# Optimization experiments

Hardware: AMD Instinct MI355X
Metric: run time of the kernel (lower is better)

## Reference

```python
import jax, jax.numpy as jnp
import numpy as np

DT = 0.05        # Euler step size
S_EULER = 2      # Euler steps between consecutive events, and after the last one (prop_to_end)


def setup_inputs() -> dict:
    key = jax.random.key(0)
    B, H, D, K, E = 512, 512, 128, 64, 256
    ks = jax.random.split(key, 16)

    def w(k, fan_in, fan_out):
        return jax.random.normal(k, (fan_in, fan_out), jnp.float32) / np.float32(np.sqrt(fan_in))

    X = jax.random.normal(ks[0], (K, E, D), jnp.float32)
    M = jax.random.bernoulli(ks[1], 0.5, (K, E, D)).astype(jnp.float32)
    # unique sample indices per event (irregular observation pattern, no scatter collisions)
    batch_idx = jax.vmap(lambda k: jax.random.permutation(k, B)[:E])(jax.random.split(ks[2], K))
    sample_idx = jnp.arange(B)
    b = lambda n: jnp.full((n,), 0.01, jnp.float32)  # torch init: bias filled with 0.01
    return {
        'X': X, 'M': M, 'batch_idx': batch_idx, 'sample_idx': sample_idx,
        'Wi': w(ks[3], D + H, H), 'bi': b(H),
        'Wf': w(ks[4], D + H, H), 'bf': b(H),
        'Wo': w(ks[5], D + H, H), 'bo': b(H),
        'Wc': w(ks[6], D + H, H), 'bc': b(H),
        'W1': w(ks[7], H, H), 'b1': b(H),
        'W2': w(ks[8], H, H), 'b2': b(H),
        'Wp1': w(ks[9], H, H), 'bp1': b(H),
        'Wp2': w(ks[10], H, D), 'bp2': b(D),
    }


def reference(X, M, batch_idx, sample_idx,
              Wi, bi, Wf, bf, Wo, bo, Wc, bc,
              W1, b1, W2, b2, Wp1, bp1, Wp2, bp2):
    B = sample_idx.shape[0]
    H = W1.shape[0]
    h0 = jnp.zeros((B, H), X.dtype)
    c0 = jnp.zeros((B, H), X.dtype)

    def euler(h):  # h <- h + dt * ODEFunc(h)
        return h + DT * (jnp.tanh(h @ W1 + b1) @ W2 + b2)

    def p_model(h):  # Linear -> ReLU -> (Dropout p=0, eval) -> Linear
        return jax.nn.relu(h @ Wp1 + bp1) @ Wp2 + bp2

    def step(carry, xs):
        h, c, loss, tot_m = carry
        Xo, Mo, idx = xs  # [E,D], [E,D], [E]
        for _ in range(S_EULER):
            h = euler(h)
        p = p_model(h)
        loss = loss + jnp.sum(jnp.abs(Xo - p[idx]) * Mo)
        tot_m = tot_m + jnp.sum(Mo)
        inp = jnp.concatenate([Xo, h[idx]], axis=-1)  # [E, D+H]
        ig = jax.nn.sigmoid(inp @ Wi + bi)
        fg = jax.nn.sigmoid(inp @ Wf + bf)
        og = jax.nn.sigmoid(inp @ Wo + bo)
        ct = jnp.tanh(inp @ Wc + bc)
        c_new = fg * c[idx] + ig * ct
        h_new = og * jnp.tanh(c_new)
        return (h.at[idx].set(h_new), c.at[idx].set(c_new), loss, tot_m), None

    init = (h0, c0, jnp.float32(0.0), jnp.float32(0.0))
    (h, c, loss, tot_m), _ = jax.lax.scan(step, init, (X, M, batch_idx))
    for _ in range(S_EULER):  # prop_to_end up to T
        h = euler(h)
    return jnp.stack([loss, loss / tot_m])
```

## Files before the change

kernel.cpp:

```cpp
#include <hip/hip_runtime.h>
#include <hip/hip_fp16.h>
#include <stdint.h>

#define Kn 64
#define En 256
#define Bn 512
#define Hn 512
#define Dn 128
#define NBLK 256
#define NTH  256
#define DT_C 0.05f


typedef _Float16 f16x8 __attribute__((ext_vector_type(8)));
typedef float    f32x4 __attribute__((ext_vector_type(4)));
typedef unsigned long long u64;

__device__ __forceinline__ float sigm(float x){ return 1.0f/(1.0f + __expf(-x)); }

__device__ __forceinline__ u64 ald(const u64* p){
  return __hip_atomic_load(p, __ATOMIC_RELAXED, __HIP_MEMORY_SCOPE_AGENT);
}
__device__ __forceinline__ void ast(u64* p, u64 v){
  __hip_atomic_store(p, v, __ATOMIC_RELAXED, __HIP_MEMORY_SCOPE_AGENT);
}

union HU { __half h[8]; u64 q[2]; uint32_t w[4]; };

__global__ void k_init(int* __restrict__ pos, float* __restrict__ acc,
                       int* __restrict__ ctr, uint32_t* __restrict__ hf){
  int i = blockIdx.x*blockDim.x + threadIdx.x;
  if (i < Kn*Bn) pos[i] = -1;
  if (i < 2) acc[i] = 0.0f;
  if (i < 1024) ctr[i] = 0;
  if (i < Hn*Hn/2) hf[i] = 0;
}

__global__ void k_scatter(const int* __restrict__ bidx, int* __restrict__ pos){
  int i = blockIdx.x*blockDim.x + threadIdx.x;
  if (i < Kn*En){
    int k = i >> 8;
    int e = i & (En-1);
    pos[(k << 9) | bidx[i]] = e;
  }
}

__global__ void k_cvt_frag(const float* __restrict__ src, __half* __restrict__ dst,
                           int KT, int N, int n){
  int i = blockIdx.x*blockDim.x + threadIdx.x;
  if (i >= n) return;
  int C = i / (KT*512);
  int r = i % (KT*512);
  int T = r >> 9;
  int q = r & 511;
  int l = q >> 3, e = q & 7;
  int srow = T*32 + ((l>>4)<<3) + e;
  int scol = C*16 + (l&15);
  dst[i] = __float2half(src[(size_t)srow*N + scol]);
}

__device__ __forceinline__ void gsync(int* c, int tgt){
  asm volatile("s_waitcnt vmcnt(0)" ::: "memory");
  __syncthreads();
  if (threadIdx.x == 0){
    __hip_atomic_fetch_add(c, 1, __ATOMIC_RELAXED, __HIP_MEMORY_SCOPE_AGENT);
    while (__hip_atomic_load(c, __ATOMIC_RELAXED, __HIP_MEMORY_SCOPE_AGENT) < tgt)
      __builtin_amdgcn_s_sleep(1);
  }
  __syncthreads();
}

__global__ __launch_bounds__(NTH, 1) void k_main(
  const float* __restrict__ X, const float* __restrict__ Mm,
  const int* __restrict__ pos, const __half* __restrict__ WF,
  __half* __restrict__ Hf, __half* __restrict__ Tf,
  const float* __restrict__ bi_, const float* __restrict__ bf_,
  const float* __restrict__ bo_, const float* __restrict__ bc_,
  const float* __restrict__ b1_, const float* __restrict__ b2_,
  const float* __restrict__ bp1_, const float* __restrict__ bp2_,
  float* __restrict__ acc, int* __restrict__ ctrbase)
{
  const __half* W1F  = WF;
  const __half* W2F  = WF + 262144;
  const __half* Wp1F = WF + 524288;
  const __half* Wp2F = WF + 786432;
  const __half* WgF  = WF + 851968;

  const int t    = threadIdx.x;
  const int bid  = blockIdx.x;
  const int s    = bid & 7;
  const int g    = bid >> 3;
  const int w    = t >> 6;
  const int lane = t & 63;

  int* ctr = ctrbase + g*32;

  __shared__ __align__(16) __half Afrag[16*512];
  __shared__ __align__(16) __half Xfrag[4*512];
  __shared__ __align__(16) float  outb[20*256];
  __shared__ float redbuf[8];

  const int row = t >> 4;
  const int q4  = t & 15;
  const int sc  = s*64 + q4*4;
  float Hreg[4] = {0,0,0,0};
  float Creg[4] = {0,0,0,0};
  float vb1[4], vb2[4], vbp1[4], vbi[4], vbf[4], vbo[4], vbc[4];
  #pragma unroll
  for (int i=0;i<4;i++){
    vb1[i]=b1_[sc+i]; vb2[i]=b2_[sc+i]; vbp1[i]=bp1_[sc+i];
    vbi[i]=bi_[sc+i]; vbf[i]=bf_[sc+i]; vbo[i]=bo_[sc+i]; vbc[i]=bc_[sc+i];
  }
  const float vbp2 = bp2_[s*16 + q4];

  f16x8 W1r[16], W2r[16], Wp1r[16];
  {
    const size_t cb = (size_t)(s*4 + w)*16*512 + lane*8;
    #pragma unroll
    for (int kt=0; kt<16; kt++){
      W1r[kt]  = *(const f16x8*)(W1F  + cb + kt*512);
      W2r[kt]  = *(const f16x8*)(W2F  + cb + kt*512);
      Wp1r[kt] = *(const f16x8*)(Wp1F + cb + kt*512);
    }
  }

  float loss_loc = 0.f, m_loc = 0.f;
  int round = 0;
  const int grow = g*16 + row;

  for (int k=0; k<Kn; k++){
    const int epos = pos[(k<<9) + grow];

    #pragma unroll 1
    for (int ph=0; ph<4; ph++){
      const __half* src = (ph & 1) ? Tf : Hf;
      {
        const int ar = t & 15, ch = t >> 4;
        const u64* sp = (const u64*)(src + ((size_t)(g*16+ar))*512 + ch*32);
        u64 v[8];
        #pragma unroll
        for (int i=0;i<8;i++) v[i] = ald(sp+i);
        #pragma unroll
        for (int kg=0;kg<4;kg++){
          u64* d = (u64*)(Afrag + ch*512 + (ar + 16*kg)*8);
          d[0] = v[2*kg]; d[1] = v[2*kg+1];
        }
      }
      __syncthreads();
      {
        f32x4 a4 = {0,0,0,0};
        if (!(ph & 1)){
          #pragma unroll
          for (int kt=0; kt<16; kt++){
            f16x8 a = *(const f16x8*)(Afrag + kt*512 + lane*8);
            a4 = __builtin_amdgcn_mfma_f32_16x16x32_f16(a, W1r[kt], a4, 0,0,0);
          }
        } else {
          #pragma unroll
          for (int kt=0; kt<16; kt++){
            f16x8 a = *(const f16x8*)(Afrag + kt*512 + lane*8);
            a4 = __builtin_amdgcn_mfma_f32_16x16x32_f16(a, W2r[kt], a4, 0,0,0);
          }
        }
        float* o = outb + w*256 + ((lane>>4)*4)*16 + (lane&15);
        o[0]=a4[0]; o[16]=a4[1]; o[32]=a4[2]; o[48]=a4[3];
      }
      __syncthreads();
      {
        const float* o = outb + (q4>>2)*256 + row*16 + (q4&3)*4;
        float v0=o[0], v1=o[1], v2=o[2], v3=o[3];
        HU u;
        if (!(ph & 1)){
          u.h[0]=__float2half(tanhf(v0+vb1[0])); u.h[1]=__float2half(tanhf(v1+vb1[1]));
          u.h[2]=__float2half(tanhf(v2+vb1[2])); u.h[3]=__float2half(tanhf(v3+vb1[3]));
          ast((u64*)(Tf + (size_t)grow*512 + sc), u.q[0]);
        } else {
          Hreg[0] += DT_C*(v0+vb2[0]); Hreg[1] += DT_C*(v1+vb2[1]);
          Hreg[2] += DT_C*(v2+vb2[2]); Hreg[3] += DT_C*(v3+vb2[3]);
          u.h[0]=__float2half(Hreg[0]); u.h[1]=__float2half(Hreg[1]);
          u.h[2]=__float2half(Hreg[2]); u.h[3]=__float2half(Hreg[3]);
          ast((u64*)(Hf + (size_t)grow*512 + sc), u.q[0]);
        }
      }
      gsync(ctr, 8*(++round));
    }

    {
      {
        const int ar = t & 15, ch = t >> 4;
        const u64* sp = (const u64*)(Hf + ((size_t)(g*16+ar))*512 + ch*32);
        u64 v[8];
        #pragma unroll
        for (int i=0;i<8;i++) v[i] = ald(sp+i);
        #pragma unroll
        for (int kg=0;kg<4;kg++){
          u64* d = (u64*)(Afrag + ch*512 + (ar + 16*kg)*8);
          d[0] = v[2*kg]; d[1] = v[2*kg+1];
        }
      }
      if (t < 64){
        const int ar = t & 15, ch = t >> 4;
        const int e = pos[(k<<9) + g*16 + ar];
        float xv[32];
        if (e >= 0){
          const float4* xp = (const float4*)(X + ((size_t)(k*En+e))*Dn + ch*32);
          #pragma unroll
          for (int i=0;i<8;i++){
            float4 f = xp[i];
            xv[4*i]=f.x; xv[4*i+1]=f.y; xv[4*i+2]=f.z; xv[4*i+3]=f.w;
          }
        } else {
          #pragma unroll
          for (int i=0;i<32;i++) xv[i]=0.f;
        }
        #pragma unroll
        for (int kg=0;kg<4;kg++){
          HU u;
          #pragma unroll
          for (int e8=0;e8<8;e8++) u.h[e8] = __float2half(xv[kg*8+e8]);
          u64* d = (u64*)(Xfrag + ch*512 + (ar + 16*kg)*8);
          d[0] = u.q[0]; d[1] = u.q[1];
        }
      }
      __syncthreads();
      {
        f32x4 a4 = {0,0,0,0};
        #pragma unroll
        for (int kt=0; kt<16; kt++){
          f16x8 a = *(const f16x8*)(Afrag + kt*512 + lane*8);
          a4 = __builtin_amdgcn_mfma_f32_16x16x32_f16(a, Wp1r[kt], a4, 0,0,0);
        }
        float* o = outb + (16+w)*256 + ((lane>>4)*4)*16 + (lane&15);
        o[0]=a4[0]; o[16]=a4[1]; o[32]=a4[2]; o[48]=a4[3];
      }
      #pragma unroll 1
      for (int i=0;i<4;i++){
        const int Cg = w*32 + s*4 + i;
        const __half* wb = WgF + (size_t)Cg*20*512;
        f32x4 a4 = {0,0,0,0};
        #pragma unroll 4
        for (int kt=0; kt<4; kt++){
          f16x8 a = *(const f16x8*)(Xfrag + kt*512 + lane*8);
          f16x8 b = *(const f16x8*)(wb + kt*512 + lane*8);
          a4 = __builtin_amdgcn_mfma_f32_16x16x32_f16(a, b, a4, 0,0,0);
        }
        #pragma unroll 4
        for (int kt=4; kt<20; kt++){
          f16x8 a = *(const f16x8*)(Afrag + (kt-4)*512 + lane*8);
          f16x8 b = *(const f16x8*)(wb + kt*512 + lane*8);
          a4 = __builtin_amdgcn_mfma_f32_16x16x32_f16(a, b, a4, 0,0,0);
        }
        float* o = outb + (w*4+i)*256 + ((lane>>4)*4)*16 + (lane&15);
        o[0]=a4[0]; o[16]=a4[1]; o[32]=a4[2]; o[48]=a4[3];
      }
      __syncthreads();
      {
        const float* o = outb + (16+(q4>>2))*256 + row*16 + (q4&3)*4;
        HU u;
        u.h[0]=__float2half(fmaxf(o[0]+vbp1[0],0.f));
        u.h[1]=__float2half(fmaxf(o[1]+vbp1[1],0.f));
        u.h[2]=__float2half(fmaxf(o[2]+vbp1[2],0.f));
        u.h[3]=__float2half(fmaxf(o[3]+vbp1[3],0.f));
        ast((u64*)(Tf + (size_t)grow*512 + sc), u.q[0]);
      }
      gsync(ctr, 8*(++round));
    }

    {
      {
        const int ar = t & 15, ch = t >> 4;
        const u64* sp = (const u64*)(Tf + ((size_t)(g*16+ar))*512 + ch*32);
        u64 v[8];
        #pragma unroll
        for (int i=0;i<8;i++) v[i] = ald(sp+i);
        #pragma unroll
        for (int kg=0;kg<4;kg++){
          u64* d = (u64*)(Afrag + ch*512 + (ar + 16*kg)*8);
          d[0] = v[2*kg]; d[1] = v[2*kg+1];
        }
      }
      __syncthreads();
      {
        const __half* wb = Wp2F + (size_t)s*16*512;
        f32x4 a4 = {0,0,0,0};
        #pragma unroll
        for (int kt2=0; kt2<4; kt2++){
          const int kt = w*4 + kt2;
          f16x8 a = *(const f16x8*)(Afrag + kt*512 + lane*8);
          f16x8 b = *(const f16x8*)(wb + kt*512 + lane*8);
          a4 = __builtin_amdgcn_mfma_f32_16x16x32_f16(a, b, a4, 0,0,0);
        }
        float* o = outb + (16+w)*256 + ((lane>>4)*4)*16 + (lane&15);
        o[0]=a4[0]; o[16]=a4[1]; o[32]=a4[2]; o[48]=a4[3];
      }
      if (epos >= 0){
        const int sub = q4 >> 2, off = row*16 + (q4&3)*4;
        const float4 pi = *(const float4*)(outb + (0*4+sub)*256 + off);
        const float4 pf = *(const float4*)(outb + (1*4+sub)*256 + off);
        const float4 po = *(const float4*)(outb + (2*4+sub)*256 + off);
        const float4 pc = *(const float4*)(outb + (3*4+sub)*256 + off);
        HU hu;
        const float gi[4]={pi.x,pi.y,pi.z,pi.w}, gf[4]={pf.x,pf.y,pf.z,pf.w};
        const float go[4]={po.x,po.y,po.z,po.w}, gc[4]={pc.x,pc.y,pc.z,pc.w};
        #pragma unroll
        for (int i=0;i<4;i++){
          float ig = sigm(gi[i] + vbi[i]);
          float fg = sigm(gf[i] + vbf[i]);
          float og = sigm(go[i] + vbo[i]);
          float ct = tanhf(gc[i] + vbc[i]);
          Creg[i] = fg*Creg[i] + ig*ct;
          Hreg[i] = og*tanhf(Creg[i]);
          hu.h[i] = __float2half(Hreg[i]);
        }
        ast((u64*)(Hf + (size_t)grow*512 + sc), hu.q[0]);
      }
      __syncthreads();
      if (epos >= 0){
        float p = outb[16*256 + row*16+q4] + outb[17*256 + row*16+q4]
                + outb[18*256 + row*16+q4] + outb[19*256 + row*16+q4] + vbp2;
        const int d = s*16 + q4;
        float xo = X[((size_t)(k*En+epos))*Dn + d];
        float mo = Mm[((size_t)(k*En+epos))*Dn + d];
        loss_loc += fabsf(xo - p)*mo;
        m_loc    += mo;
      }
      gsync(ctr, 8*(++round));
    }
  }

  #pragma unroll
  for (int off=32; off>0; off>>=1){
    loss_loc += __shfl_down(loss_loc, off);
    m_loc    += __shfl_down(m_loc, off);
  }
  if (lane == 0){ redbuf[w] = loss_loc; redbuf[4+w] = m_loc; }
  __syncthreads();
  if (t == 0){
    atomicAdd(acc+0, redbuf[0]+redbuf[1]+redbuf[2]+redbuf[3]);
    atomicAdd(acc+1, redbuf[4]+redbuf[5]+redbuf[6]+redbuf[7]);
  }
}

__global__ void k_fin(const float* __restrict__ acc, float* __restrict__ out){
  if (threadIdx.x == 0){
    out[0] = acc[0];
    out[1] = acc[0]/acc[1];
  }
}

extern "C" void kernel_launch(void* const* d_in, const int* in_sizes, int n_in,
                              void* d_out, int out_size, void* d_ws, size_t ws_size,
                              hipStream_t stream)
{
  const float* X   = (const float*)d_in[0];
  const float* Mm  = (const float*)d_in[1];
  const int*  bidx = (const int*)d_in[2];
  const float* Wi  = (const float*)d_in[4];
  const float* bi  = (const float*)d_in[5];
  const float* Wf  = (const float*)d_in[6];
  const float* bff = (const float*)d_in[7];
  const float* Wo  = (const float*)d_in[8];
  const float* bo  = (const float*)d_in[9];
  const float* Wc  = (const float*)d_in[10];
  const float* bc  = (const float*)d_in[11];
  const float* W1  = (const float*)d_in[12];
  const float* b1  = (const float*)d_in[13];
  const float* W2  = (const float*)d_in[14];
  const float* b2  = (const float*)d_in[15];
  const float* Wp1 = (const float*)d_in[16];
  const float* bp1 = (const float*)d_in[17];
  const float* Wp2 = (const float*)d_in[18];
  const float* bp2 = (const float*)d_in[19];

  char* ws = (char*)d_ws;
  int*    pos = (int*)ws;
  float*  acc = (float*)(ws + 131072);
  int*    ctr = (int*)(ws + 131200);
  __half* Hf  = (__half*)(ws + 1048576);
  __half* Tf  = (__half*)(ws + 1572864);
  __half* WF  = (__half*)(ws + 4194304);

  k_init   <<<512, 256, 0, stream>>>(pos, acc, ctr, (uint32_t*)Hf);
  k_scatter<<<(Kn*En + 255)/256, 256, 0, stream>>>(bidx, pos);

  k_cvt_frag<<<(262144+255)/256, 256, 0, stream>>>(W1,  WF,          16, 512, 262144);
  k_cvt_frag<<<(262144+255)/256, 256, 0, stream>>>(W2,  WF + 262144, 16, 512, 262144);
  k_cvt_frag<<<(262144+255)/256, 256, 0, stream>>>(Wp1, WF + 524288, 16, 512, 262144);
  k_cvt_frag<<<(65536 +255)/256, 256, 0, stream>>>(Wp2, WF + 786432, 16, 128, 65536);
  k_cvt_frag<<<(327680+255)/256, 256, 0, stream>>>(Wi,  WF + 851968,            20, 512, 327680);
  k_cvt_frag<<<(327680+255)/256, 256, 0, stream>>>(Wf,  WF + 851968 + 327680,   20, 512, 327680);
  k_cvt_frag<<<(327680+255)/256, 256, 0, stream>>>(Wo,  WF + 851968 + 655360,   20, 512, 327680);
  k_cvt_frag<<<(327680+255)/256, 256, 0, stream>>>(Wc,  WF + 851968 + 983040,   20, 512, 327680);

  k_main<<<NBLK, NTH, 0, stream>>>(X, Mm, pos, WF, Hf, Tf,
                                   bi, bff, bo, bc, b1, b2, bp1, bp2, acc, ctr);
  k_fin<<<1, 64, 0, stream>>>(acc, (float*)d_out);
}
```

Measured before the change: 1.916 ms.

## Split batch rows over twice as many blocks and use per-block flag barriers

Doubles the persistent grid to 512 blocks, each handling 8 batch rows instead of 16 (the MFMA tiles are padded with zero rows), and sets launch bounds to allow two blocks per CU. The per-group atomic-counter barrier is replaced by per-block flag slots that each block writes and eight threads poll. The aim is more latency hiding across two co-resident blocks and less contention on one shared counter. In exchange, half of every MFMA does no useful work and register pressure rises, since each block still keeps three weight matrices in registers and the launch bound now targets two blocks per CU.

```diff
diff --git a/kernel.cpp b/kernel.cpp
--- a/kernel.cpp
+++ b/kernel.cpp
@@ -7,7 +7,7 @@
 #define Bn 512
 #define Hn 512
 #define Dn 128
-#define NBLK 256
+#define NBLK 512
 #define NTH  256
 #define DT_C 0.05f
 
@@ -28,11 +28,11 @@
 union HU { __half h[8]; u64 q[2]; uint32_t w[4]; };
 
 __global__ void k_init(int* __restrict__ pos, float* __restrict__ acc,
-                       int* __restrict__ ctr, uint32_t* __restrict__ hf){
+                       int* __restrict__ flg, uint32_t* __restrict__ hf){
   int i = blockIdx.x*blockDim.x + threadIdx.x;
   if (i < Kn*Bn) pos[i] = -1;
   if (i < 2) acc[i] = 0.0f;
-  if (i < 1024) ctr[i] = 0;
+  if (i < 64*8*32) flg[i] = 0;
   if (i < Hn*Hn/2) hf[i] = 0;
 }
 
@@ -59,18 +59,20 @@
   dst[i] = __float2half(src[(size_t)srow*N + scol]);
 }
 
-__device__ __forceinline__ void gsync(int* c, int tgt){
+__device__ __forceinline__ void gsync(int* flgbase, int slot, int r){
   asm volatile("s_waitcnt vmcnt(0)" ::: "memory");
   __syncthreads();
-  if (threadIdx.x == 0){
-    __hip_atomic_fetch_add(c, 1, __ATOMIC_RELAXED, __HIP_MEMORY_SCOPE_AGENT);
-    while (__hip_atomic_load(c, __ATOMIC_RELAXED, __HIP_MEMORY_SCOPE_AGENT) < tgt)
-      __builtin_amdgcn_s_sleep(1);
+  if (threadIdx.x == 0)
+    __hip_atomic_store(flgbase + slot*32, r, __ATOMIC_RELAXED, __HIP_MEMORY_SCOPE_AGENT);
+  if (threadIdx.x < 8){
+    while (__hip_atomic_load(flgbase + threadIdx.x*32, __ATOMIC_RELAXED,
+                             __HIP_MEMORY_SCOPE_AGENT) < r)
+      __builtin_amdgcn_s_sleep(2);
   }
   __syncthreads();
 }
 
-__global__ __launch_bounds__(NTH, 1) void k_main(
+__global__ __launch_bounds__(NTH, 2) void k_main(
   const float* __restrict__ X, const float* __restrict__ Mm,
   const int* __restrict__ pos, const __half* __restrict__ WF,
   __half* __restrict__ Hf, __half* __restrict__ Tf,
@@ -78,7 +80,7 @@
   const float* __restrict__ bo_, const float* __restrict__ bc_,
   const float* __restrict__ b1_, const float* __restrict__ b2_,
   const float* __restrict__ bp1_, const float* __restrict__ bp2_,
-  float* __restrict__ acc, int* __restrict__ ctrbase)
+  float* __restrict__ acc, int* __restrict__ flgall)
 {
   const __half* W1F  = WF;
   const __half* W2F  = WF + 262144;
@@ -93,7 +95,7 @@
   const int w    = t >> 6;
   const int lane = t & 63;
 
-  int* ctr = ctrbase + g*32;
+  int* flgbase = flgall + g*8*32;
 
   __shared__ __align__(16) __half Afrag[16*512];
   __shared__ __align__(16) __half Xfrag[4*512];
@@ -126,20 +128,25 @@
 
   float loss_loc = 0.f, m_loc = 0.f;
   int round = 0;
-  const int grow = g*16 + row;
+  const int grow = g*8 + row;
 
   for (int k=0; k<Kn; k++){
-    const int epos = pos[(k<<9) + grow];
+    const int epos = (row < 8) ? pos[(k<<9) + grow] : -1;
 
     #pragma unroll 1
     for (int ph=0; ph<4; ph++){
       const __half* src = (ph & 1) ? Tf : Hf;
       {
         const int ar = t & 15, ch = t >> 4;
-        const u64* sp = (const u64*)(src + ((size_t)(g*16+ar))*512 + ch*32);
         u64 v[8];
-        #pragma unroll
-        for (int i=0;i<8;i++) v[i] = ald(sp+i);
+        if (ar < 8){
+          const u64* sp = (const u64*)(src + ((size_t)(g*8+ar))*512 + ch*32);
+          #pragma unroll
+          for (int i=0;i<8;i++) v[i] = ald(sp+i);
+        } else {
+          #pragma unroll
+          for (int i=0;i<8;i++) v[i] = 0;
+        }
         #pragma unroll
         for (int kg=0;kg<4;kg++){
           u64* d = (u64*)(Afrag + ch*512 + (ar + 16*kg)*8);
@@ -166,7 +173,7 @@
         o[0]=a4[0]; o[16]=a4[1]; o[32]=a4[2]; o[48]=a4[3];
       }
       __syncthreads();
-      {
+      if (row < 8){
         const float* o = outb + (q4>>2)*256 + row*16 + (q4&3)*4;
         float v0=o[0], v1=o[1], v2=o[2], v3=o[3];
         HU u;
@@ -182,16 +189,21 @@
           ast((u64*)(Hf + (size_t)grow*512 + sc), u.q[0]);
         }
       }
-      gsync(ctr, 8*(++round));
+      gsync(flgbase, s, ++round);
     }
 
     {
       {
         const int ar = t & 15, ch = t >> 4;
-        const u64* sp = (const u64*)(Hf + ((size_t)(g*16+ar))*512 + ch*32);
         u64 v[8];
-        #pragma unroll
-        for (int i=0;i<8;i++) v[i] = ald(sp+i);
+        if (ar < 8){
+          const u64* sp = (const u64*)(Hf + ((size_t)(g*8+ar))*512 + ch*32);
+          #pragma unroll
+          for (int i=0;i<8;i++) v[i] = ald(sp+i);
+        } else {
+          #pragma unroll
+          for (int i=0;i<8;i++) v[i] = 0;
+        }
         #pragma unroll
         for (int kg=0;kg<4;kg++){
           u64* d = (u64*)(Afrag + ch*512 + (ar + 16*kg)*8);
@@ -200,7 +212,7 @@
       }
       if (t < 64){
         const int ar = t & 15, ch = t >> 4;
-        const int e = pos[(k<<9) + g*16 + ar];
+        const int e = (ar < 8) ? pos[(k<<9) + g*8 + ar] : -1;
         float xv[32];
         if (e >= 0){
           const float4* xp = (const float4*)(X + ((size_t)(k*En+e))*Dn + ch*32);
@@ -254,7 +266,7 @@
         o[0]=a4[0]; o[16]=a4[1]; o[32]=a4[2]; o[48]=a4[3];
       }
       __syncthreads();
-      {
+      if (row < 8){
         const float* o = outb + (16+(q4>>2))*256 + row*16 + (q4&3)*4;
         HU u;
         u.h[0]=__float2half(fmaxf(o[0]+vbp1[0],0.f));
@@ -263,16 +275,21 @@
         u.h[3]=__float2half(fmaxf(o[3]+vbp1[3],0.f));
         ast((u64*)(Tf + (size_t)grow*512 + sc), u.q[0]);
       }
-      gsync(ctr, 8*(++round));
+      gsync(flgbase, s, ++round);
     }
 
     {
       {
         const int ar = t & 15, ch = t >> 4;
-        const u64* sp = (const u64*)(Tf + ((size_t)(g*16+ar))*512 + ch*32);
         u64 v[8];
-        #pragma unroll
-        for (int i=0;i<8;i++) v[i] = ald(sp+i);
+        if (ar < 8){
+          const u64* sp = (const u64*)(Tf + ((size_t)(g*8+ar))*512 + ch*32);
+          #pragma unroll
+          for (int i=0;i<8;i++) v[i] = ald(sp+i);
+        } else {
+          #pragma unroll
+          for (int i=0;i<8;i++) v[i] = 0;
+        }
         #pragma unroll
         for (int kg=0;kg<4;kg++){
           u64* d = (u64*)(Afrag + ch*512 + (ar + 16*kg)*8);
@@ -324,7 +341,7 @@
         loss_loc += fabsf(xo - p)*mo;
         m_loc    += mo;
       }
-      gsync(ctr, 8*(++round));
+      gsync(flgbase, s, ++round);
     }
   }
 
@@ -375,12 +392,12 @@
   char* ws = (char*)d_ws;
   int*    pos = (int*)ws;
   float*  acc = (float*)(ws + 131072);
-  int*    ctr = (int*)(ws + 131200);
+  int*    flg = (int*)(ws + 196608);
   __half* Hf  = (__half*)(ws + 1048576);
   __half* Tf  = (__half*)(ws + 1572864);
   __half* WF  = (__half*)(ws + 4194304);
 
-  k_init   <<<512, 256, 0, stream>>>(pos, acc, ctr, (uint32_t*)Hf);
+  k_init   <<<512, 256, 0, stream>>>(pos, acc, flg, (uint32_t*)Hf);
   k_scatter<<<(Kn*En + 255)/256, 256, 0, stream>>>(bidx, pos);
 
   k_cvt_frag<<<(262144+255)/256, 256, 0, stream>>>(W1,  WF,          16, 512, 262144);
@@ -393,6 +410,6 @@
   k_cvt_frag<<<(327680+255)/256, 256, 0, stream>>>(Wc,  WF + 851968 + 983040,   20, 512, 327680);
 
   k_main<<<NBLK, NTH, 0, stream>>>(X, Mm, pos, WF, Hf, Tf,
-                                   bi, bff, bo, bc, b1, b2, bp1, bp2, acc, ctr);
+                                   bi, bff, bo, bc, b1, b2, bp1, bp2, acc, flg);
   k_fin<<<1, 64, 0, stream>>>(acc, (float*)d_out);
 }
```

Result: slower. 2.867 ms (+49.6%).

## Use 64 persistent blocks with 64-row tiles and per-block flag sync

Applied to the files above, without the earlier changes.

Cuts the persistent grid from 256 to 64 blocks. Each block now handles 64 batch rows (four 16-row chunks) instead of 16, so every weight fragment feeds four MFMA accumulators. The group-wide counter barrier is replaced by per-block flags: each block publishes a round number and polls the flags of the 32 blocks it depends on. Results are stored straight from MFMA accumulators as half-precision atomics, without a shared-memory round trip. Gate GEMMs now run right after publishing and overlap with the next phase's wait, and the LSTM update moves into the following phase. This trades fewer CUs and more work per block for fewer barriers and better reuse of the weight registers.

```diff
diff --git a/kernel.cpp b/kernel.cpp
--- a/kernel.cpp
+++ b/kernel.cpp
@@ -7,7 +7,7 @@
 #define Bn 512
 #define Hn 512
 #define Dn 128
-#define NBLK 256
+#define NBLK 64
 #define NTH  256
 #define DT_C 0.05f
 
@@ -21,18 +21,19 @@
 __device__ __forceinline__ u64 ald(const u64* p){
   return __hip_atomic_load(p, __ATOMIC_RELAXED, __HIP_MEMORY_SCOPE_AGENT);
 }
-__device__ __forceinline__ void ast(u64* p, u64 v){
-  __hip_atomic_store(p, v, __ATOMIC_RELAXED, __HIP_MEMORY_SCOPE_AGENT);
-}
-
-union HU { __half h[8]; u64 q[2]; uint32_t w[4]; };
+__device__ __forceinline__ void ash(__half* p, float v){
+  __hip_atomic_store((unsigned short*)p, __half_as_ushort(__float2half(v)),
+                     __ATOMIC_RELAXED, __HIP_MEMORY_SCOPE_AGENT);
+}
+
+union HU { __half h[8]; u64 q[2]; };
 
 __global__ void k_init(int* __restrict__ pos, float* __restrict__ acc,
-                       int* __restrict__ ctr, uint32_t* __restrict__ hf){
+                       int* __restrict__ flg, uint32_t* __restrict__ hf){
   int i = blockIdx.x*blockDim.x + threadIdx.x;
   if (i < Kn*Bn) pos[i] = -1;
   if (i < 2) acc[i] = 0.0f;
-  if (i < 1024) ctr[i] = 0;
+  if (i < 32*8*32) flg[i] = 0;
   if (i < Hn*Hn/2) hf[i] = 0;
 }
 
@@ -59,17 +60,6 @@
   dst[i] = __float2half(src[(size_t)srow*N + scol]);
 }
 
-__device__ __forceinline__ void gsync(int* c, int tgt){
-  asm volatile("s_waitcnt vmcnt(0)" ::: "memory");
-  __syncthreads();
-  if (threadIdx.x == 0){
-    __hip_atomic_fetch_add(c, 1, __ATOMIC_RELAXED, __HIP_MEMORY_SCOPE_AGENT);
-    while (__hip_atomic_load(c, __ATOMIC_RELAXED, __HIP_MEMORY_SCOPE_AGENT) < tgt)
-      __builtin_amdgcn_s_sleep(1);
-  }
-  __syncthreads();
-}
-
 __global__ __launch_bounds__(NTH, 1) void k_main(
   const float* __restrict__ X, const float* __restrict__ Mm,
   const int* __restrict__ pos, const __half* __restrict__ WF,
@@ -78,7 +68,7 @@
   const float* __restrict__ bo_, const float* __restrict__ bc_,
   const float* __restrict__ b1_, const float* __restrict__ b2_,
   const float* __restrict__ bp1_, const float* __restrict__ bp2_,
-  float* __restrict__ acc, int* __restrict__ ctrbase)
+  float* __restrict__ acc, int* __restrict__ flg)
 {
   const __half* W1F  = WF;
   const __half* W2F  = WF + 262144;
@@ -89,118 +79,133 @@
   const int t    = threadIdx.x;
   const int bid  = blockIdx.x;
   const int s    = bid & 7;
-  const int g    = bid >> 3;
+  const int qg   = bid >> 3;
   const int w    = t >> 6;
   const int lane = t & 63;
-
-  int* ctr = ctrbase + g*32;
-
-  __shared__ __align__(16) __half Afrag[16*512];
-  __shared__ __align__(16) __half Xfrag[4*512];
-  __shared__ __align__(16) float  outb[20*256];
+  const int cl   = lane & 15;
+  const int rq   = lane >> 4;
+  const int jc   = s*64 + w*16 + cl;
+  const int q4   = t & 15, lrow = t >> 4;
+
+  __shared__ __align__(16) __half Af[4][8192];
+  __shared__ __align__(16) __half Xf[4][2048];
+  __shared__ __align__(16) float  outb[1024];
   __shared__ float redbuf[8];
 
-  const int row = t >> 4;
-  const int q4  = t & 15;
-  const int sc  = s*64 + q4*4;
-  float Hreg[4] = {0,0,0,0};
-  float Creg[4] = {0,0,0,0};
-  float vb1[4], vb2[4], vbp1[4], vbi[4], vbf[4], vbo[4], vbc[4];
-  #pragma unroll
-  for (int i=0;i<4;i++){
-    vb1[i]=b1_[sc+i]; vb2[i]=b2_[sc+i]; vbp1[i]=bp1_[sc+i];
-    vbi[i]=bi_[sc+i]; vbf[i]=bf_[sc+i]; vbo[i]=bo_[sc+i]; vbc[i]=bc_[sc+i];
-  }
-  const float vbp2 = bp2_[s*16 + q4];
-
-  f16x8 W1r[16], W2r[16], Wp1r[16];
+  f16x8 W1r[16], W2r[16], wp2r[4];
   {
-    const size_t cb = (size_t)(s*4 + w)*16*512 + lane*8;
+    const size_t cb = (size_t)(s*4 + w)*16*512 + (size_t)lane*8;
     #pragma unroll
     for (int kt=0; kt<16; kt++){
-      W1r[kt]  = *(const f16x8*)(W1F  + cb + kt*512);
-      W2r[kt]  = *(const f16x8*)(W2F  + cb + kt*512);
-      Wp1r[kt] = *(const f16x8*)(Wp1F + cb + kt*512);
+      W1r[kt] = *(const f16x8*)(W1F + cb + kt*512);
+      W2r[kt] = *(const f16x8*)(W2F + cb + kt*512);
     }
-  }
-
-  float loss_loc = 0.f, m_loc = 0.f;
-  int round = 0;
-  const int grow = g*16 + row;
+    #pragma unroll
+    for (int j=0;j<4;j++)
+      wp2r[j] = *(const f16x8*)(Wp2F + (size_t)(s*16 + w*4 + j)*512 + (size_t)lane*8);
+  }
+
+  float Hreg[4][4], Creg[4][4];
+  #pragma unroll
+  for (int c=0;c<4;c++)
+    #pragma unroll
+    for (int r=0;r<4;r++){ Hreg[c][r]=0.f; Creg[c][r]=0.f; }
+
+  const float vb1=b1_[jc], vb2=b2_[jc], vbp1=bp1_[jc];
+  const float vbi=bi_[jc], vbf=bf_[jc], vbo=bo_[jc], vbc=bc_[jc];
+  const float vbp2 = bp2_[s*16 + q4];
+
+  f32x4 gacc[4][4];
+  float loss_loc=0.f, m_loc=0.f;
+  int rnd = 0;
+
+#define POLLW() do{                                                          \
+    if (t < 32){                                                             \
+      int* fp = flg + ((qg*4 + (t>>3))*8 + (t&7))*32;                        \
+      while (__hip_atomic_load(fp, __ATOMIC_RELAXED,                         \
+                               __HIP_MEMORY_SCOPE_AGENT) < rnd)              \
+        __builtin_amdgcn_s_sleep(1);                                         \
+    }                                                                        \
+    __syncthreads();                                                         \
+  }while(0)
+
+#define PUBLISHW() do{                                                       \
+    asm volatile("s_waitcnt vmcnt(0)" ::: "memory");                         \
+    __syncthreads();                                                         \
+    if (t < 4)                                                               \
+      __hip_atomic_store(flg + ((qg*4 + t)*8 + s)*32, rnd+1,                 \
+                         __ATOMIC_RELAXED, __HIP_MEMORY_SCOPE_AGENT);        \
+    rnd++;                                                                   \
+  }while(0)
+
+#define STAGE_ALL(SRC) do{                                                   \
+    const int ar = t & 15, ch = t >> 4;                                      \
+    _Pragma("unroll")                                                        \
+    for (int c=0;c<4;c++){                                                   \
+      const u64* sp = (const u64*)((SRC) +                                   \
+          ((size_t)((qg*4+c)*16 + ar))*512 + ch*32);                         \
+      u64 v[8];                                                              \
+      _Pragma("unroll")                                                      \
+      for (int i=0;i<8;i++) v[i] = ald(sp+i);                                \
+      _Pragma("unroll")                                                      \
+      for (int kg=0;kg<4;kg++){                                              \
+        u64* d = (u64*)(&Af[c][ch*512 + (ar+16*kg)*8]);                      \
+        d[0] = v[2*kg]; d[1] = v[2*kg+1];                                    \
+      }                                                                      \
+    }                                                                        \
+  }while(0)
 
   for (int k=0; k<Kn; k++){
-    const int epos = pos[(k<<9) + grow];
-
     #pragma unroll 1
     for (int ph=0; ph<4; ph++){
-      const __half* src = (ph & 1) ? Tf : Hf;
+      POLLW();
+      const __half* srcb = (ph & 1) ? Tf : Hf;
+      STAGE_ALL(srcb);
+      __syncthreads();
+      f32x4 a4[4];
+      #pragma unroll
+      for (int c=0;c<4;c++) a4[c] = (f32x4){0.f,0.f,0.f,0.f};
+      if (!(ph & 1)){
+        #pragma unroll
+        for (int kt=0; kt<16; kt++)
+          #pragma unroll
+          for (int c=0;c<4;c++){
+            f16x8 a = *(const f16x8*)(&Af[c][kt*512 + lane*8]);
+            a4[c] = __builtin_amdgcn_mfma_f32_16x16x32_f16(a, W1r[kt], a4[c], 0,0,0);
+          }
+        #pragma unroll
+        for (int c=0;c<4;c++)
+          #pragma unroll
+          for (int r=0;r<4;r++){
+            const size_t grow = (size_t)((qg*4+c)*16 + rq*4 + r);
+            ash(Tf + grow*512 + jc, tanhf(a4[c][r] + vb1));
+          }
+      } else {
+        #pragma unroll
+        for (int kt=0; kt<16; kt++)
+          #pragma unroll
+          for (int c=0;c<4;c++){
+            f16x8 a = *(const f16x8*)(&Af[c][kt*512 + lane*8]);
+            a4[c] = __builtin_amdgcn_mfma_f32_16x16x32_f16(a, W2r[kt], a4[c], 0,0,0);
+          }
+        #pragma unroll
+        for (int c=0;c<4;c++)
+          #pragma unroll
+          for (int r=0;r<4;r++){
+            Hreg[c][r] += DT_C*(a4[c][r] + vb2);
+            const size_t grow = (size_t)((qg*4+c)*16 + rq*4 + r);
+            ash(Hf + grow*512 + jc, Hreg[c][r]);
+          }
+      }
+      PUBLISHW();
+    }
+
+    {
+      POLLW();
+      STAGE_ALL(Hf);
       {
-        const int ar = t & 15, ch = t >> 4;
-        const u64* sp = (const u64*)(src + ((size_t)(g*16+ar))*512 + ch*32);
-        u64 v[8];
-        #pragma unroll
-        for (int i=0;i<8;i++) v[i] = ald(sp+i);
-        #pragma unroll
-        for (int kg=0;kg<4;kg++){
-          u64* d = (u64*)(Afrag + ch*512 + (ar + 16*kg)*8);
-          d[0] = v[2*kg]; d[1] = v[2*kg+1];
-        }
-      }
-      __syncthreads();
-      {
-        f32x4 a4 = {0,0,0,0};
-        if (!(ph & 1)){
-          #pragma unroll
-          for (int kt=0; kt<16; kt++){
-            f16x8 a = *(const f16x8*)(Afrag + kt*512 + lane*8);
-            a4 = __builtin_amdgcn_mfma_f32_16x16x32_f16(a, W1r[kt], a4, 0,0,0);
-          }
-        } else {
-          #pragma unroll
-          for (int kt=0; kt<16; kt++){
-            f16x8 a = *(const f16x8*)(Afrag + kt*512 + lane*8);
-            a4 = __builtin_amdgcn_mfma_f32_16x16x32_f16(a, W2r[kt], a4, 0,0,0);
-          }
-        }
-        float* o = outb + w*256 + ((lane>>4)*4)*16 + (lane&15);
-        o[0]=a4[0]; o[16]=a4[1]; o[32]=a4[2]; o[48]=a4[3];
-      }
-      __syncthreads();
-      {
-        const float* o = outb + (q4>>2)*256 + row*16 + (q4&3)*4;
-        float v0=o[0], v1=o[1], v2=o[2], v3=o[3];
-        HU u;
-        if (!(ph & 1)){
-          u.h[0]=__float2half(tanhf(v0+vb1[0])); u.h[1]=__float2half(tanhf(v1+vb1[1]));
-          u.h[2]=__float2half(tanhf(v2+vb1[2])); u.h[3]=__float2half(tanhf(v3+vb1[3]));
-          ast((u64*)(Tf + (size_t)grow*512 + sc), u.q[0]);
-        } else {
-          Hreg[0] += DT_C*(v0+vb2[0]); Hreg[1] += DT_C*(v1+vb2[1]);
-          Hreg[2] += DT_C*(v2+vb2[2]); Hreg[3] += DT_C*(v3+vb2[3]);
-          u.h[0]=__float2half(Hreg[0]); u.h[1]=__float2half(Hreg[1]);
-          u.h[2]=__float2half(Hreg[2]); u.h[3]=__float2half(Hreg[3]);
-          ast((u64*)(Hf + (size_t)grow*512 + sc), u.q[0]);
-        }
-      }
-      gsync(ctr, 8*(++round));
-    }
-
-    {
-      {
-        const int ar = t & 15, ch = t >> 4;
-        const u64* sp = (const u64*)(Hf + ((size_t)(g*16+ar))*512 + ch*32);
-        u64 v[8];
-        #pragma unroll
-        for (int i=0;i<8;i++) v[i] = ald(sp+i);
-        #pragma unroll
-        for (int kg=0;kg<4;kg++){
-          u64* d = (u64*)(Afrag + ch*512 + (ar + 16*kg)*8);
-          d[0] = v[2*kg]; d[1] = v[2*kg+1];
-        }
-      }
-      if (t < 64){
-        const int ar = t & 15, ch = t >> 4;
-        const int e = pos[(k<<9) + g*16 + ar];
+        const int ar = lane & 15, ch = lane >> 4;
+        const int e = pos[(k<<9) + (qg*4 + w)*16 + ar];
         float xv[32];
         if (e >= 0){
           const float4* xp = (const float4*)(X + ((size_t)(k*En+e))*Dn + ch*32);
@@ -218,113 +223,112 @@
           HU u;
           #pragma unroll
           for (int e8=0;e8<8;e8++) u.h[e8] = __float2half(xv[kg*8+e8]);
-          u64* d = (u64*)(Xfrag + ch*512 + (ar + 16*kg)*8);
+          u64* d = (u64*)(&Xf[w][ch*512 + (ar+16*kg)*8]);
           d[0] = u.q[0]; d[1] = u.q[1];
         }
       }
       __syncthreads();
-      {
-        f32x4 a4 = {0,0,0,0};
-        #pragma unroll
-        for (int kt=0; kt<16; kt++){
-          f16x8 a = *(const f16x8*)(Afrag + kt*512 + lane*8);
-          a4 = __builtin_amdgcn_mfma_f32_16x16x32_f16(a, Wp1r[kt], a4, 0,0,0);
-        }
-        float* o = outb + (16+w)*256 + ((lane>>4)*4)*16 + (lane&15);
+      f32x4 p1[4];
+      #pragma unroll
+      for (int c=0;c<4;c++) p1[c] = (f32x4){0.f,0.f,0.f,0.f};
+      #pragma unroll
+      for (int half=0; half<2; half++){
+        f16x8 wp1h[8];
+        #pragma unroll
+        for (int j=0;j<8;j++)
+          wp1h[j] = *(const f16x8*)(Wp1F +
+              (size_t)((s*4+w)*16 + half*8 + j)*512 + (size_t)lane*8);
+        #pragma unroll
+        for (int j=0;j<8;j++){
+          const int kt = half*8 + j;
+          #pragma unroll
+          for (int c=0;c<4;c++){
+            f16x8 a = *(const f16x8*)(&Af[c][kt*512 + lane*8]);
+            p1[c] = __builtin_amdgcn_mfma_f32_16x16x32_f16(a, wp1h[j], p1[c], 0,0,0);
+          }
+        }
+      }
+      #pragma unroll
+      for (int c=0;c<4;c++)
+        #pragma unroll
+        for (int r=0;r<4;r++){
+          const size_t grow = (size_t)((qg*4+c)*16 + rq*4 + r);
+          ash(Tf + grow*512 + jc, fmaxf(p1[c][r] + vbp1, 0.f));
+        }
+      PUBLISHW();
+      if (k < Kn-1){
+        #pragma unroll
+        for (int g4=0; g4<4; g4++){
+          #pragma unroll
+          for (int c=0;c<4;c++) gacc[c][g4] = (f32x4){0.f,0.f,0.f,0.f};
+          #pragma unroll
+          for (int half=0; half<2; half++){
+            f16x8 gw[10];
+            const __half* gb = WgF + (size_t)g4*327680 +
+                (size_t)((s*4+w)*20 + half*10)*512 + (size_t)lane*8;
+            #pragma unroll
+            for (int j=0;j<10;j++) gw[j] = *(const f16x8*)(gb + j*512);
+            #pragma unroll
+            for (int j=0;j<10;j++){
+              const int kt = half*10 + j;
+              #pragma unroll
+              for (int c=0;c<4;c++){
+                f16x8 a = (kt < 4)
+                  ? *(const f16x8*)(&Xf[c][kt*512 + lane*8])
+                  : *(const f16x8*)(&Af[c][(kt-4)*512 + lane*8]);
+                gacc[c][g4] = __builtin_amdgcn_mfma_f32_16x16x32_f16(a, gw[j], gacc[c][g4], 0,0,0);
+              }
+            }
+          }
+        }
+      }
+    }
+
+    {
+      POLLW();
+      STAGE_ALL(Tf);
+      __syncthreads();
+      if (k < Kn-1){
+        #pragma unroll
+        for (int c=0;c<4;c++)
+          #pragma unroll
+          for (int r=0;r<4;r++){
+            const int sr = rq*4 + r;
+            const int er = pos[(k<<9) + (qg*4+c)*16 + sr];
+            if (er >= 0){
+              float ig = sigm(gacc[c][0][r] + vbi);
+              float fg = sigm(gacc[c][1][r] + vbf);
+              float og = sigm(gacc[c][2][r] + vbo);
+              float ct = tanhf(gacc[c][3][r] + vbc);
+              Creg[c][r] = fg*Creg[c][r] + ig*ct;
+              Hreg[c][r] = og*tanhf(Creg[c][r]);
+              ash(Hf + ((size_t)((qg*4+c)*16 + sr))*512 + jc, Hreg[c][r]);
+            }
+          }
+      }
+      PUBLISHW();
+      #pragma unroll 1
+      for (int c=0;c<4;c++){
+        f32x4 a4 = {0.f,0.f,0.f,0.f};
+        #pragma unroll
+        for (int j=0;j<4;j++){
+          f16x8 a = *(const f16x8*)(&Af[c][(w*4+j)*512 + lane*8]);
+          a4 = __builtin_amdgcn_mfma_f32_16x16x32_f16(a, wp2r[j], a4, 0,0,0);
+        }
+        float* o = outb + w*256 + (rq*4)*16 + cl;
         o[0]=a4[0]; o[16]=a4[1]; o[32]=a4[2]; o[48]=a4[3];
-      }
-      #pragma unroll 1
-      for (int i=0;i<4;i++){
-        const int Cg = w*32 + s*4 + i;
-        const __half* wb = WgF + (size_t)Cg*20*512;
-        f32x4 a4 = {0,0,0,0};
-        #pragma unroll 4
-        for (int kt=0; kt<4; kt++){
-          f16x8 a = *(const f16x8*)(Xfrag + kt*512 + lane*8);
-          f16x8 b = *(const f16x8*)(wb + kt*512 + lane*8);
-          a4 = __builtin_amdgcn_mfma_f32_16x16x32_f16(a, b, a4, 0,0,0);
-        }
-        #pragma unroll 4
-        for (int kt=4; kt<20; kt++){
-          f16x8 a = *(const f16x8*)(Afrag + (kt-4)*512 + lane*8);
-          f16x8 b = *(const f16x8*)(wb + kt*512 + lane*8);
-          a4 = __builtin_amdgcn_mfma_f32_16x16x32_f16(a, b, a4, 0,0,0);
-        }
-        float* o = outb + (w*4+i)*256 + ((lane>>4)*4)*16 + (lane&15);
-        o[0]=a4[0]; o[16]=a4[1]; o[32]=a4[2]; o[48]=a4[3];
-      }
-      __syncthreads();
-      {
-        const float* o = outb + (16+(q4>>2))*256 + row*16 + (q4&3)*4;
-        HU u;
-        u.h[0]=__float2half(fmaxf(o[0]+vbp1[0],0.f));
-        u.h[1]=__float2half(fmaxf(o[1]+vbp1[1],0.f));
-        u.h[2]=__float2half(fmaxf(o[2]+vbp1[2],0.f));
-        u.h[3]=__float2half(fmaxf(o[3]+vbp1[3],0.f));
-        ast((u64*)(Tf + (size_t)grow*512 + sc), u.q[0]);
-      }
-      gsync(ctr, 8*(++round));
-    }
-
-    {
-      {
-        const int ar = t & 15, ch = t >> 4;
-        const u64* sp = (const u64*)(Tf + ((size_t)(g*16+ar))*512 + ch*32);
-        u64 v[8];
-        #pragma unroll
-        for (int i=0;i<8;i++) v[i] = ald(sp+i);
-        #pragma unroll
-        for (int kg=0;kg<4;kg++){
-          u64* d = (u64*)(Afrag + ch*512 + (ar + 16*kg)*8);
-          d[0] = v[2*kg]; d[1] = v[2*kg+1];
-        }
-      }
-      __syncthreads();
-      {
-        const __half* wb = Wp2F + (size_t)s*16*512;
-        f32x4 a4 = {0,0,0,0};
-        #pragma unroll
-        for (int kt2=0; kt2<4; kt2++){
-          const int kt = w*4 + kt2;
-          f16x8 a = *(const f16x8*)(Afrag + kt*512 + lane*8);
-          f16x8 b = *(const f16x8*)(wb + kt*512 + lane*8);
-          a4 = __builtin_amdgcn_mfma_f32_16x16x32_f16(a, b, a4, 0,0,0);
-        }
-        float* o = outb + (16+w)*256 + ((lane>>4)*4)*16 + (lane&15);
-        o[0]=a4[0]; o[16]=a4[1]; o[32]=a4[2]; o[48]=a4[3];
-      }
-      if (epos >= 0){
-        const int sub = q4 >> 2, off = row*16 + (q4&3)*4;
-        const float4 pi = *(const float4*)(outb + (0*4+sub)*256 + off);
-        const float4 pf = *(const float4*)(outb + (1*4+sub)*256 + off);
-        const float4 po = *(const float4*)(outb + (2*4+sub)*256 + off);
-        const float4 pc = *(const float4*)(outb + (3*4+sub)*256 + off);
-        HU hu;
-        const float gi[4]={pi.x,pi.y,pi.z,pi.w}, gf[4]={pf.x,pf.y,pf.z,pf.w};
-        const float go[4]={po.x,po.y,po.z,po.w}, gc[4]={pc.x,pc.y,pc.z,pc.w};
-        #pragma unroll
-        for (int i=0;i<4;i++){
-          float ig = sigm(gi[i] + vbi[i]);
-          float fg = sigm(gf[i] + vbf[i]);
-          float og = sigm(go[i] + vbo[i]);
-          float ct = tanhf(gc[i] + vbc[i]);
-          Creg[i] = fg*Creg[i] + ig*ct;
-          Hreg[i] = og*tanhf(Creg[i]);
-          hu.h[i] = __float2half(Hreg[i]);
-        }
-        ast((u64*)(Hf + (size_t)grow*512 + sc), hu.q[0]);
-      }
-      __syncthreads();
-      if (epos >= 0){
-        float p = outb[16*256 + row*16+q4] + outb[17*256 + row*16+q4]
-                + outb[18*256 + row*16+q4] + outb[19*256 + row*16+q4] + vbp2;
-        const int d = s*16 + q4;
-        float xo = X[((size_t)(k*En+epos))*Dn + d];
-        float mo = Mm[((size_t)(k*En+epos))*Dn + d];
-        loss_loc += fabsf(xo - p)*mo;
-        m_loc    += mo;
-      }
-      gsync(ctr, 8*(++round));
+        __syncthreads();
+        const int el = pos[(k<<9) + (qg*4+c)*16 + lrow];
+        if (el >= 0){
+          float p = outb[lrow*16+q4] + outb[256+lrow*16+q4]
+                  + outb[512+lrow*16+q4] + outb[768+lrow*16+q4] + vbp2;
+          const size_t xoff = ((size_t)(k*En+el))*Dn + s*16 + q4;
+          float xo = X[xoff], mo = Mm[xoff];
+          loss_loc += fabsf(xo - p)*mo;
+          m_loc    += mo;
+        }
+        __syncthreads();
+      }
     }
   }
 
@@ -339,6 +343,9 @@
     atomicAdd(acc+0, redbuf[0]+redbuf[1]+redbuf[2]+redbuf[3]);
     atomicAdd(acc+1, redbuf[4]+redbuf[5]+redbuf[6]+redbuf[7]);
   }
+#undef POLLW
+#undef PUBLISHW
+#undef STAGE_ALL
 }
 
 __global__ void k_fin(const float* __restrict__ acc, float* __restrict__ out){
@@ -375,12 +382,12 @@
   char* ws = (char*)d_ws;
   int*    pos = (int*)ws;
   float*  acc = (float*)(ws + 131072);
-  int*    ctr = (int*)(ws + 131200);
+  int*    flg = (int*)(ws + 196608);
   __half* Hf  = (__half*)(ws + 1048576);
   __half* Tf  = (__half*)(ws + 1572864);
   __half* WF  = (__half*)(ws + 4194304);
 
-  k_init   <<<512, 256, 0, stream>>>(pos, acc, ctr, (uint32_t*)Hf);
+  k_init   <<<512, 256, 0, stream>>>(pos, acc, flg, (uint32_t*)Hf);
   k_scatter<<<(Kn*En + 255)/256, 256, 0, stream>>>(bidx, pos);
 
   k_cvt_frag<<<(262144+255)/256, 256, 0, stream>>>(W1,  WF,          16, 512, 262144);
@@ -393,6 +400,6 @@
   k_cvt_frag<<<(327680+255)/256, 256, 0, stream>>>(Wc,  WF + 851968 + 983040,   20, 512, 327680);
 
   k_main<<<NBLK, NTH, 0, stream>>>(X, Mm, pos, WF, Hf, Tf,
-                                   bi, bff, bo, bc, b1, b2, bp1, bp2, acc, ctr);
+                                   bi, bff, bo, bc, b1, b2, bp1, bp2, acc, flg);
   k_fin<<<1, 64, 0, stream>>>(acc, (float*)d_out);
 }
```

Measured after the change: 5.596 ms. 192% more time.
